# Optimization experiments

Hardware: AMD Instinct MI355X
Metric: run time of the kernel (lower is better)

Reference implementation:

```python
import jax, jax.numpy as jnp
import numpy as np

B, S, DIM, H, HD = 2, 2048, 512, 8, 64
VD = DIM // H  # 64
QK = H * HD


def setup_inputs() -> dict:
    key = jax.random.key(0)
    k1, k2, k3, k4, k5 = jax.random.split(key, 5)
    x = jax.random.normal(k1, (B, S, DIM), dtype=jnp.float32)
    mask = jax.random.bernoulli(k2, 0.5, (B, S))
    # per-position rotation matrices, scaled to keep activations O(1)
    rotator = jax.random.normal(k3, (B, S, HD, HD), dtype=jnp.float32) / np.sqrt(HD)
    # torch Linear weights: [out_features, in_features], no bias
    W_trans = jax.random.normal(k4, (2 * QK + DIM, DIM), dtype=jnp.float32) / np.sqrt(DIM)
    W_o = jax.random.normal(k5, (DIM, DIM), dtype=jnp.float32) / np.sqrt(DIM)
    return {"x": x, "mask": mask, "rotator": rotator, "W_trans": W_trans, "W_o": W_o}


def _taylor_attention(qs, ks, vs, mask):
    # 2nd-order Taylor approximation of exp for softmax weights
    # qs/ks: [B,S,H,HD], vs: [B,S,H,VD], mask: [B,S] key mask
    scores = jnp.einsum('bqhd,bkhd->bhqk', qs, ks) / np.sqrt(HD)
    w = 1.0 + scores + 0.5 * scores * scores
    w = jnp.where(mask[:, None, None, :], w, 0.0)
    w = w / jnp.sum(w, axis=-1, keepdims=True)
    out = jnp.einsum('bhqk,bkhd->bqhd', w, vs)
    return out.reshape(out.shape[0], out.shape[1], -1)  # [B,S,DIM]


def reference(x, mask, rotator, W_trans, W_o):
    t = x @ W_trans.T  # [B,S,2*QK+DIM]
    qs = t[..., :QK].reshape(B, S, H, HD)
    ks = t[..., QK:2 * QK].reshape(B, S, H, HD)
    vs = t[..., 2 * QK:].reshape(B, S, H, VD)
    sel = mask[..., None, None]
    qs = jnp.where(sel, jnp.einsum('bsij,bshj->bshi', rotator, qs), qs)
    ks = jnp.where(sel, jnp.einsum('bsij,bshj->bshi', rotator, ks), ks)
    out = _taylor_attention(qs, ks, vs, mask)
    return out @ W_o.T
```

## Files before the change

### kernel.cpp

```cpp
#include <hip/hip_runtime.h>
#include <hip/hip_bf16.h>

#define B_    2
#define S_    2048
#define DIM_  512
#define H_    8
#define HD_   64
#define TOUT_ 1536
#define ROWS_ (B_ * S_)

typedef unsigned short ushort_t;
typedef __attribute__((ext_vector_type(8))) __bf16 bf16x8;
typedef __attribute__((ext_vector_type(4))) float floatx4;

#define AS_GLB __attribute__((address_space(1)))
#define AS_LDS __attribute__((address_space(3)))

__device__ __forceinline__ unsigned short f2bfu(float f) {
    unsigned u = __float_as_uint(f);
    unsigned r = (u + 0x7fffu + ((u >> 16) & 1u)) >> 16;
    return (unsigned short)r;
}
__device__ __forceinline__ bf16x8 cvt8(const float* p) {
    float4 a = *reinterpret_cast<const float4*>(p);
    float4 b = *reinterpret_cast<const float4*>(p + 4);
    ushort_t o[8] = {f2bfu(a.x), f2bfu(a.y), f2bfu(a.z), f2bfu(a.w),
                     f2bfu(b.x), f2bfu(b.y), f2bfu(b.z), f2bfu(b.w)};
    return *reinterpret_cast<bf16x8*>(o);
}

#define XN4_  (ROWS_ * DIM_ / 4)
#define WTN4_ (TOUT_ * DIM_ / 4)
#define WON4_ (DIM_ * DIM_ / 4)
#define CASTBLKS_ ((XN4_ + WTN4_ + WON4_) / 256)
__global__ __launch_bounds__(256) void prep_inputs(const float* __restrict__ x,
                                                   const float* __restrict__ wt,
                                                   const float* __restrict__ wo,
                                                   const unsigned char* __restrict__ mb,
                                                   ushort_t* __restrict__ xb,
                                                   ushort_t* __restrict__ wtb,
                                                   ushort_t* __restrict__ wob,
                                                   int* __restrict__ wm) {
    if (blockIdx.x >= CASTBLKS_) {
        __shared__ int s_bf, s_f, s_u8;
        int tid = threadIdx.x;
        if (tid == 0) { s_bf = 0; s_f = 0; s_u8 = 0; }
        __syncthreads();
        int cbf = 0, cf = 0, cu8 = 0;
        for (int i = tid; i < 4096; i += 256) {
            unsigned char v = mb[i];
            if (v == 0x3F || v == 0x80) {
                cf++;
                if ((i & 3) == 1) cbf++;
            } else if (v != 0 && (i & 3) != 0) {
                cu8++;
            }
        }
        atomicAdd(&s_bf, cbf); atomicAdd(&s_f, cf); atomicAdd(&s_u8, cu8);
        __syncthreads();
        int cls = (s_bf > 0) ? 2 : (s_f > 0) ? 3 : (s_u8 > 0) ? 0 : 1;
        for (int i = tid; i < ROWS_; i += 256) {
            int v;
            if (cls == 0)      v = (mb[i] != 0);
            else if (cls == 1) v = (reinterpret_cast<const int*>(mb)[i] != 0);
            else if (cls == 2) v = ((reinterpret_cast<const unsigned short*>(mb)[i] & 0x7fffu) != 0);
            else               v = ((reinterpret_cast<const unsigned int*>(mb)[i] & 0x7fffffffu) != 0);
            wm[i] = v;
        }
        return;
    }
    int i = blockIdx.x * 256 + threadIdx.x;
    const float* s; ushort_t* d; int off;
    if (i < XN4_)              { s = x;  d = xb;  off = i; }
    else if (i < XN4_ + WTN4_) { s = wt; d = wtb; off = i - XN4_; }
    else                       { s = wo; d = wob; off = i - XN4_ - WTN4_; }
    float4 v = reinterpret_cast<const float4*>(s)[off];
    ushort_t o[4] = {f2bfu(v.x), f2bfu(v.y), f2bfu(v.z), f2bfu(v.w)};
    reinterpret_cast<uint2*>(d)[off] = *reinterpret_cast<uint2*>(o);
}

template <int TM, int N, int K, bool OUT_BF16>
__global__ __launch_bounds__(256) void mfma_gemm_bt(const ushort_t* __restrict__ A,
                                                    const ushort_t* __restrict__ Bm,
                                                    void* __restrict__ Cout) {
    constexpr int FM = (TM + 31) / 32;
    __shared__ __align__(16) ushort_t As[TM * 64];
    __shared__ __align__(16) ushort_t Bs[128 * 64];
    int tid = threadIdx.x;
    int lane = tid & 63;
    int wv = tid >> 6;
    int wm = wv >> 1, wn = wv & 1;
    int quad = lane >> 4;
    int mrow = lane & 15;
    int bx = blockIdx.x;
    int by = blockIdx.y;

    floatx4 acc[FM][4];
#pragma unroll
    for (int i = 0; i < FM; i++)
#pragma unroll
        for (int j = 0; j < 4; j++) acc[i][j] = (floatx4){0.f, 0.f, 0.f, 0.f};

    for (int k0 = 0; k0 < K; k0 += 64) {
#pragma unroll
        for (int t = 0; t < TM / 32; t++) {
            int p = (wv * (TM / 32) + t) * 64 + lane;
            int row = p >> 3, cp = p & 7;
            int gc = cp ^ (row & 7);
            const ushort_t* ga = A + (size_t)(by * TM + row) * K + k0 + gc * 8;
            __builtin_amdgcn_global_load_lds((const AS_GLB unsigned int*)ga,
                                             (AS_LDS unsigned int*)&As[(size_t)(wv * (TM / 32) + t) * 64 * 8],
                                             16, 0, 0);
        }
#pragma unroll
        for (int t = 0; t < 4; t++) {
            int p = (wv * 4 + t) * 64 + lane;
            int row = p >> 3, cp = p & 7;
            int gc = cp ^ (row & 7);
            const ushort_t* gb = Bm + (size_t)(bx * 128 + row) * K + k0 + gc * 8;
            __builtin_amdgcn_global_load_lds((const AS_GLB unsigned int*)gb,
                                             (AS_LDS unsigned int*)&Bs[(size_t)(wv * 4 + t) * 64 * 8],
                                             16, 0, 0);
        }
        __syncthreads();
#pragma unroll
        for (int ks = 0; ks < 64; ks += 32) {
            int c = (ks >> 3) + quad;
            bf16x8 af[FM], bf[4];
#pragma unroll
            for (int i = 0; i < FM; i++) {
                int row = wm * (TM / 2) + i * 16 + mrow;
                int pos = row * 8 + (c ^ (row & 7));
                af[i] = *reinterpret_cast<const bf16x8*>(&As[pos * 8]);
            }
#pragma unroll
            for (int j = 0; j < 4; j++) {
                int row = wn * 64 + j * 16 + mrow;
                int pos = row * 8 + (c ^ (row & 7));
                bf[j] = *reinterpret_cast<const bf16x8*>(&Bs[pos * 8]);
            }
#pragma unroll
            for (int i = 0; i < FM; i++)
#pragma unroll
                for (int j = 0; j < 4; j++)
                    acc[i][j] = __builtin_amdgcn_mfma_f32_16x16x32_bf16(af[i], bf[j], acc[i][j], 0, 0, 0);
        }
        __syncthreads();
    }

    int col0 = bx * 128 + wn * 64 + mrow;
    int row0 = by * TM + wm * (TM / 2) + quad * 4;
    if constexpr (OUT_BF16) {
        ushort_t* C = reinterpret_cast<ushort_t*>(Cout);
#pragma unroll
        for (int i = 0; i < FM; i++)
#pragma unroll
            for (int j = 0; j < 4; j++)
#pragma unroll
                for (int r = 0; r < 4; r++)
                    C[(size_t)(row0 + i * 16 + r) * N + col0 + j * 16] = f2bfu(acc[i][j][r]);
    } else {
        float* C = reinterpret_cast<float*>(Cout);
#pragma unroll
        for (int i = 0; i < FM; i++)
#pragma unroll
            for (int j = 0; j < 4; j++)
#pragma unroll
                for (int r = 0; r < 4; r++)
                    C[(size_t)(row0 + i * 16 + r) * N + col0 + j * 16] = acc[i][j][r];
    }
}

__global__ __launch_bounds__(256) void rot_qk_mfma(const ushort_t* __restrict__ t,
                                                   const float* __restrict__ rotG,
                                                   const int* __restrict__ wm,
                                                   ushort_t* __restrict__ Qb,
                                                   ushort_t* __restrict__ Kb) {
    int lane = threadIdx.x & 63;
    int wv = threadIdx.x >> 6;
    int row = blockIdx.x * 4 + wv;
    int b = row >> 11, s = row & 2047;
    int lm = lane & 15, quad = lane >> 4;
    const ushort_t* trow = t + (size_t)row * TOUT_;
    int kb = s >> 4, l = s & 15;

    if (wm[row]) {
        bf16x8 af[2];
#pragma unroll
        for (int kc = 0; kc < 2; kc++)
            af[kc] = *reinterpret_cast<const bf16x8*>(trow + lm * 64 + kc * 32 + quad * 8);

        const float* R = rotG + (size_t)row * 4096;
        floatx4 dacc[4];
#pragma unroll
        for (int nb = 0; nb < 4; nb++) dacc[nb] = (floatx4){0.f, 0.f, 0.f, 0.f};
#pragma unroll
        for (int nb = 0; nb < 4; nb++)
#pragma unroll
            for (int kc = 0; kc < 2; kc++) {
                bf16x8 bfr = cvt8(R + (size_t)(nb * 16 + lm) * 64 + kc * 32 + quad * 8);
                dacc[nb] = __builtin_amdgcn_mfma_f32_16x16x32_bf16(af[kc], bfr, dacc[nb], 0, 0, 0);
            }
#pragma unroll
        for (int nb = 0; nb < 4; nb++)
#pragma unroll
            for (int r = 0; r < 4; r++) {
                int vec = quad * 4 + r;
                int hh = vec & 7;
                ushort_t v = f2bfu(dacc[nb][r]);
                if (vec >= 8) {
                    int c = nb * 2 + (lm >> 3), e = lm & 7;
                    Kb[(((size_t)(b * 8 + hh) * 128 + kb) * 8 + c) * 128 + l * 8 + e] = v;
                } else {
                    Qb[((size_t)(b * 8 + hh) * 2048 + s) * 64 + nb * 16 + lm] = v;
                }
            }
    } else {
#pragma unroll
        for (int nb = 0; nb < 4; nb++)
#pragma unroll
            for (int r = 0; r < 4; r++) {
                int vec = quad * 4 + r;
                int hh = vec & 7;
                ushort_t v = trow[vec * 64 + nb * 16 + lm];
                if (vec >= 8) {
                    int c = nb * 2 + (lm >> 3), e = lm & 7;
                    Kb[(((size_t)(b * 8 + hh) * 128 + kb) * 8 + c) * 128 + l * 8 + e] = v;
                } else {
                    Qb[((size_t)(b * 8 + hh) * 2048 + s) * 64 + nb * 16 + lm] = v;
                }
            }
    }
}

__global__ __launch_bounds__(256) void prep_vt(const ushort_t* __restrict__ t,
                                               const int* __restrict__ wm,
                                               ushort_t* __restrict__ VtF) {
    __shared__ ushort_t tile[64][72];
    __shared__ ushort_t umask[64];
    int st = blockIdx.x;
    int bh = blockIdx.y;
    int b = bh >> 3, h = bh & 7;
    int tid = threadIdx.x;
    if (tid < 64) umask[tid] = wm[b * 2048 + st * 64 + tid] ? 0xFFFFu : 0u;
#pragma unroll
    for (int i = 0; i < 2; i++) {
        int q = i * 256 + tid;
        int r = q >> 3, c8 = (q & 7) * 8;
        uint4 v = *reinterpret_cast<const uint4*>(
            t + (size_t)(b * 2048 + st * 64 + r) * TOUT_ + 1024 + h * 64 + c8);
        *reinterpret_cast<uint4*>(&tile[r][c8]) = v;
    }
    __syncthreads();
    {
        int dn = tid >> 6, quad = (tid >> 4) & 3, lm = tid & 15;
#pragma unroll
        for (int jj = 0; jj < 2; jj++) {
            ushort_t o[8];
#pragma unroll
            for (int e = 0; e < 8; e++) {
                int key = jj * 32 + ((e >> 2) << 4) + quad * 4 + (e & 3);
                o[e] = (ushort_t)(tile[key][dn * 16 + lm] & umask[key]);
            }
            size_t base = (((((size_t)(bh * 32 + st) * 5 + dn) * 2 + jj) * 4 + quad) * 16 + lm) * 8;
            *reinterpret_cast<uint4*>(VtF + base) = *reinterpret_cast<const uint4*>(o);
        }
    }
    if (tid < 64) {
        int quad = tid >> 4, lm = tid & 15;
#pragma unroll
        for (int jj = 0; jj < 2; jj++) {
            ushort_t o[8];
#pragma unroll
            for (int e = 0; e < 8; e++) {
                int key = jj * 32 + ((e >> 2) << 4) + quad * 4 + (e & 3);
                o[e] = (lm == 0) ? (umask[key] ? (ushort_t)0x3F80u : (ushort_t)0u) : (ushort_t)0u;
            }
            size_t base = (((((size_t)(bh * 32 + st) * 5 + 4) * 2 + jj) * 4 + quad) * 16 + lm) * 8;
            *reinterpret_cast<uint4*>(VtF + base) = *reinterpret_cast<const uint4*>(o);
        }
    }
}

__global__ __launch_bounds__(256) void tmha_attn_mfma(const ushort_t* __restrict__ Qb,
                                                      const ushort_t* __restrict__ KbF,
                                                      const ushort_t* __restrict__ VtF,
                                                      ushort_t* __restrict__ attnAb) {
    int tid = threadIdx.x;
    int lane = tid & 63;
    int wv = tid >> 6;
    int lm = lane & 15;
    int quad = lane >> 4;

    int bid = blockIdx.x;
    int w = ((bid & 7) << 6) | (bid >> 3);
    int qt = w & 31;
    int bh = w >> 5;
    int b = bh >> 3, h = bh & 7;

    const ushort_t* Kf = KbF + (size_t)bh * 128 * 1024;
    const ushort_t* Vf = VtF + (size_t)bh * 163840;

    bf16x8 qf[2];
    {
        const ushort_t* qp = Qb + ((size_t)bh * 2048 + qt * 64 + wv * 16 + lm) * 64 + quad * 8;
        qf[0] = *reinterpret_cast<const bf16x8*>(qp);
        qf[1] = *reinterpret_cast<const bf16x8*>(qp + 32);
    }

    floatx4 zero4 = (floatx4){0.f, 0.f, 0.f, 0.f};
    floatx4 oacc[5];
#pragma unroll
    for (int j = 0; j < 5; j++) oacc[j] = zero4;

    bf16x8 kr[4][2];
    bf16x8 vr[5][2];
    auto loadK = [&](int kt) {
        int kb = kt >> 4;
#pragma unroll
        for (int j = 0; j < 4; j++)
#pragma unroll
            for (int kc = 0; kc < 2; kc++)
                kr[j][kc] = *reinterpret_cast<const bf16x8*>(
                    Kf + (((size_t)(kb + j) * 8 + kc * 4 + quad) * 16 + lm) * 8);
    };
    auto loadV = [&](int kt) {
        const ushort_t* p = Vf + (size_t)(kt >> 6) * 5120 + quad * 128 + lm * 8;
#pragma unroll
        for (int dn = 0; dn < 5; dn++)
#pragma unroll
            for (int jj = 0; jj < 2; jj++)
                vr[dn][jj] = *reinterpret_cast<const bf16x8*>(p + dn * 1024 + jj * 512);
    };

    loadK(0); loadV(0);
#pragma unroll 1
    for (int tt = 0; tt < 32; tt++) {
        int ktn = (tt == 31) ? 0 : (tt + 1) * 64;

        floatx4 sacc[4];
        __builtin_amdgcn_s_setprio(1);
#pragma unroll
        for (int j = 0; j < 4; j++) {
            sacc[j] = __builtin_amdgcn_mfma_f32_16x16x32_bf16(kr[j][0], qf[0], zero4, 0, 0, 0);
            sacc[j] = __builtin_amdgcn_mfma_f32_16x16x32_bf16(kr[j][1], qf[1], sacc[j], 0, 0, 0);
        }
        __builtin_amdgcn_s_setprio(0);

        loadK(ktn);

        bf16x8 pa8[2];
#pragma unroll
        for (int jj = 0; jj < 2; jj++) {
            ushort_t o[8];
#pragma unroll
            for (int half = 0; half < 2; half++)
#pragma unroll
                for (int r = 0; r < 4; r++) {
                    float s = sacc[2 * jj + half][r];
                    float wgt = fmaf(s, fmaf(s, 0.0078125f, 0.125f), 1.0f);
                    o[half * 4 + r] = f2bfu(wgt);
                }
            pa8[jj] = *reinterpret_cast<bf16x8*>(o);
        }

        __builtin_amdgcn_s_setprio(1);
#pragma unroll
        for (int jj = 0; jj < 2; jj++)
#pragma unroll
            for (int dn = 0; dn < 5; dn++)
                oacc[dn] = __builtin_amdgcn_mfma_f32_16x16x32_bf16(pa8[jj], vr[dn][jj], oacc[dn], 0, 0, 0);
        __builtin_amdgcn_s_setprio(0);

        loadV(ktn);
    }

    float inv[4];
#pragma unroll
    for (int r = 0; r < 4; r++) {
        float dn = __shfl(oacc[4][r], lane & 48);
        inv[r] = 1.0f / dn;
    }
#pragma unroll
    for (int dn = 0; dn < 4; dn++)
#pragma unroll
        for (int r = 0; r < 4; r++) {
            int qrow = b * 2048 + qt * 64 + wv * 16 + quad * 4 + r;
            attnAb[(size_t)qrow * DIM_ + h * 64 + dn * 16 + lm] = f2bfu(oacc[dn][r] * inv[r]);
        }
}

extern "C" void kernel_launch(void* const* d_in, const int* in_sizes, int n_in,
                              void* d_out, int out_size, void* d_ws, size_t ws_size,
                              hipStream_t stream) {
    (void)in_sizes; (void)n_in; (void)out_size; (void)ws_size;
    const float* x    = (const float*)d_in[0];
    const void*  mask = d_in[1];
    const float* rot  = (const float*)d_in[2];
    const float* Wt   = (const float*)d_in[3];
    const float* Wo   = (const float*)d_in[4];

    char* ws = (char*)d_ws;
    int* wmask       = (int*)(ws + 64);
    ushort_t* t      = (ushort_t*)(ws + 32768);
    ushort_t* Xb     = (ushort_t*)(ws + 12615680);
    ushort_t* Wtb    = (ushort_t*)(ws + 16809984);
    ushort_t* Wob    = (ushort_t*)(ws + 18382848);
    ushort_t* Qb     = (ushort_t*)(ws + 18907136);
    ushort_t* Kb     = (ushort_t*)(ws + 23101440);
    ushort_t* VtF    = (ushort_t*)(ws + 27295744);
    ushort_t* attnAb = (ushort_t*)(ws + 32538624);

    prep_inputs<<<CASTBLKS_ + 1, 256, 0, stream>>>(x, Wt, Wo, (const unsigned char*)mask,
                                                   Xb, Wtb, Wob, wmask);

    {
        dim3 grid(TOUT_ / 128, ROWS_ / 64);
        mfma_gemm_bt<64, TOUT_, DIM_, true><<<grid, 256, 0, stream>>>(Xb, Wtb, (void*)t);
    }

    rot_qk_mfma<<<ROWS_ / 4, 256, 0, stream>>>(t, rot, wmask, Qb, Kb);

    {
        dim3 grid(32, 16);
        prep_vt<<<grid, 256, 0, stream>>>(t, wmask, VtF);
    }

    tmha_attn_mfma<<<512, 256, 0, stream>>>(Qb, Kb, VtF, attnAb);

    {
        dim3 grid(DIM_ / 128, ROWS_ / 32);
        mfma_gemm_bt<32, DIM_, DIM_, false><<<grid, 256, 0, stream>>>(attnAb, Wob, d_out);
    }
}
```

Before: 195.2 us.

## Double-buffer K/V tile prefetch and move mask column to compact buffer

```diff
diff --git a/kernel.cpp b/kernel.cpp
--- a/kernel.cpp
+++ b/kernel.cpp
@@ -235,7 +235,8 @@
 
 __global__ __launch_bounds__(256) void prep_vt(const ushort_t* __restrict__ t,
                                                const int* __restrict__ wm,
-                                               ushort_t* __restrict__ VtF) {
+                                               ushort_t* __restrict__ VtF,
+                                               ushort_t* __restrict__ MfF) {
     __shared__ ushort_t tile[64][72];
     __shared__ ushort_t umask[64];
     int st = blockIdx.x;
@@ -262,29 +263,27 @@
                 int key = jj * 32 + ((e >> 2) << 4) + quad * 4 + (e & 3);
                 o[e] = (ushort_t)(tile[key][dn * 16 + lm] & umask[key]);
             }
-            size_t base = (((((size_t)(bh * 32 + st) * 5 + dn) * 2 + jj) * 4 + quad) * 16 + lm) * 8;
+            size_t base = (((((size_t)(bh * 32 + st) * 4 + dn) * 2 + jj) * 4 + quad) * 16 + lm) * 8;
             *reinterpret_cast<uint4*>(VtF + base) = *reinterpret_cast<const uint4*>(o);
         }
     }
-    if (tid < 64) {
-        int quad = tid >> 4, lm = tid & 15;
-#pragma unroll
-        for (int jj = 0; jj < 2; jj++) {
-            ushort_t o[8];
-#pragma unroll
-            for (int e = 0; e < 8; e++) {
-                int key = jj * 32 + ((e >> 2) << 4) + quad * 4 + (e & 3);
-                o[e] = (lm == 0) ? (umask[key] ? (ushort_t)0x3F80u : (ushort_t)0u) : (ushort_t)0u;
-            }
-            size_t base = (((((size_t)(bh * 32 + st) * 5 + 4) * 2 + jj) * 4 + quad) * 16 + lm) * 8;
-            *reinterpret_cast<uint4*>(VtF + base) = *reinterpret_cast<const uint4*>(o);
-        }
+    if (tid < 8) {
+        int jj = tid >> 2, quad = tid & 3;
+        ushort_t o[8];
+#pragma unroll
+        for (int e = 0; e < 8; e++) {
+            int key = jj * 32 + ((e >> 2) << 4) + quad * 4 + (e & 3);
+            o[e] = umask[key] ? (ushort_t)0x3F80u : (ushort_t)0u;
+        }
+        size_t base = (((size_t)(bh * 32 + st) * 2 + jj) * 4 + quad) * 8;
+        *reinterpret_cast<uint4*>(MfF + base) = *reinterpret_cast<const uint4*>(o);
     }
 }
 
 __global__ __launch_bounds__(256) void tmha_attn_mfma(const ushort_t* __restrict__ Qb,
                                                       const ushort_t* __restrict__ KbF,
                                                       const ushort_t* __restrict__ VtF,
+                                                      const ushort_t* __restrict__ MfF,
                                                       ushort_t* __restrict__ attnAb) {
     int tid = threadIdx.x;
     int lane = tid & 63;
@@ -298,8 +297,9 @@
     int bh = w >> 5;
     int b = bh >> 3, h = bh & 7;
 
-    const ushort_t* Kf = KbF + (size_t)bh * 128 * 1024;
-    const ushort_t* Vf = VtF + (size_t)bh * 163840;
+    const ushort_t* Kf = KbF + (size_t)bh * 131072;
+    const ushort_t* Vf = VtF + (size_t)bh * 131072;
+    const ushort_t* Mf = MfF + (size_t)bh * 2048;
 
     bf16x8 qf[2];
     {
@@ -309,34 +309,39 @@
     }
 
     floatx4 zero4 = (floatx4){0.f, 0.f, 0.f, 0.f};
+    bf16x8 vzero;
+    *reinterpret_cast<uint4*>(&vzero) = (uint4){0u, 0u, 0u, 0u};
     floatx4 oacc[5];
 #pragma unroll
     for (int j = 0; j < 5; j++) oacc[j] = zero4;
 
-    bf16x8 kr[4][2];
-    bf16x8 vr[5][2];
-    auto loadK = [&](int kt) {
-        int kb = kt >> 4;
+    bf16x8 kA[4][2], kB[4][2], vA[4][2], vB[4][2], mA[2], mB[2];
+
+    auto loadK = [&](bf16x8 (&kr)[4][2], int tt) {
+        const ushort_t* p = Kf + (size_t)(tt & 31) * 4096 + quad * 128 + lm * 8;
 #pragma unroll
         for (int j = 0; j < 4; j++)
 #pragma unroll
             for (int kc = 0; kc < 2; kc++)
-                kr[j][kc] = *reinterpret_cast<const bf16x8*>(
-                    Kf + (((size_t)(kb + j) * 8 + kc * 4 + quad) * 16 + lm) * 8);
+                kr[j][kc] = *reinterpret_cast<const bf16x8*>(p + (j * 8 + kc * 4) * 128);
     };
-    auto loadV = [&](int kt) {
-        const ushort_t* p = Vf + (size_t)(kt >> 6) * 5120 + quad * 128 + lm * 8;
-#pragma unroll
-        for (int dn = 0; dn < 5; dn++)
+    auto loadV = [&](bf16x8 (&vr)[4][2], int tt) {
+        const ushort_t* p = Vf + (size_t)(tt & 31) * 4096 + quad * 128 + lm * 8;
+#pragma unroll
+        for (int dn = 0; dn < 4; dn++)
 #pragma unroll
             for (int jj = 0; jj < 2; jj++)
                 vr[dn][jj] = *reinterpret_cast<const bf16x8*>(p + dn * 1024 + jj * 512);
     };
-
-    loadK(0); loadV(0);
-#pragma unroll 1
-    for (int tt = 0; tt < 32; tt++) {
-        int ktn = (tt == 31) ? 0 : (tt + 1) * 64;
+    auto loadM = [&](bf16x8 (&mf)[2], int tt) {
+        const ushort_t* p = Mf + (size_t)(tt & 31) * 64 + quad * 8;
+        mf[0] = *reinterpret_cast<const bf16x8*>(p);
+        mf[1] = *reinterpret_cast<const bf16x8*>(p + 32);
+    };
+
+    auto step = [&](bf16x8 (&kr)[4][2], bf16x8 (&vr)[4][2], bf16x8 (&mf)[2],
+                    bf16x8 (&krN)[4][2], bf16x8 (&vrN)[4][2], bf16x8 (&mfN)[2], int tpre) {
+        __builtin_amdgcn_s_barrier();
 
         floatx4 sacc[4];
         __builtin_amdgcn_s_setprio(1);
@@ -347,7 +352,7 @@
         }
         __builtin_amdgcn_s_setprio(0);
 
-        loadK(ktn);
+        loadK(krN, tpre);
 
         bf16x8 pa8[2];
 #pragma unroll
@@ -366,13 +371,24 @@
 
         __builtin_amdgcn_s_setprio(1);
 #pragma unroll
-        for (int jj = 0; jj < 2; jj++)
-#pragma unroll
-            for (int dn = 0; dn < 5; dn++)
+        for (int jj = 0; jj < 2; jj++) {
+#pragma unroll
+            for (int dn = 0; dn < 4; dn++)
                 oacc[dn] = __builtin_amdgcn_mfma_f32_16x16x32_bf16(pa8[jj], vr[dn][jj], oacc[dn], 0, 0, 0);
+            bf16x8 vb = (lm == 0) ? mf[jj] : vzero;
+            oacc[4] = __builtin_amdgcn_mfma_f32_16x16x32_bf16(pa8[jj], vb, oacc[4], 0, 0, 0);
+        }
         __builtin_amdgcn_s_setprio(0);
 
-        loadV(ktn);
+        loadV(vrN, tpre); loadM(mfN, tpre);
+    };
+
+    loadK(kA, 0); loadV(vA, 0); loadM(mA, 0);
+    loadK(kB, 1); loadV(vB, 1); loadM(mB, 1);
+#pragma unroll 1
+    for (int it = 0; it < 16; it++) {
+        step(kA, vA, mA, kA, vA, mA, 2 * it + 2);
+        step(kB, vB, mB, kB, vB, mB, 2 * it + 3);
     }
 
     float inv[4];
@@ -409,7 +425,8 @@
     ushort_t* Qb     = (ushort_t*)(ws + 18907136);
     ushort_t* Kb     = (ushort_t*)(ws + 23101440);
     ushort_t* VtF    = (ushort_t*)(ws + 27295744);
-    ushort_t* attnAb = (ushort_t*)(ws + 32538624);
+    ushort_t* MfF    = (ushort_t*)(ws + 31490048);
+    ushort_t* attnAb = (ushort_t*)(ws + 31555584);
 
     prep_inputs<<<CASTBLKS_ + 1, 256, 0, stream>>>(x, Wt, Wo, (const unsigned char*)mask,
                                                    Xb, Wtb, Wob, wmask);
@@ -423,10 +440,10 @@
 
     {
         dim3 grid(32, 16);
-        prep_vt<<<grid, 256, 0, stream>>>(t, wmask, VtF);
-    }
-
-    tmha_attn_mfma<<<512, 256, 0, stream>>>(Qb, Kb, VtF, attnAb);
+        prep_vt<<<grid, 256, 0, stream>>>(t, wmask, VtF, MfF);
+    }
+
+    tmha_attn_mfma<<<512, 256, 0, stream>>>(Qb, Kb, VtF, MfF, attnAb);
 
     {
         dim3 grid(DIM_ / 128, ROWS_ / 32);
```

New measurement: 192.1 us. Within noise of the previous version (-1.6%).
